# Kernel tuning notes

Hardware: AMD Instinct MI355X
Metric: run time of the kernel (lower is better)

## Reference

```python
import jax, jax.numpy as jnp
import numpy as np
from math import log

D_MODEL = 512
MAX_LEN = 2048
B, S = 32, 2048


def make_pe(max_len, d_model):
    position = np.arange(max_len, dtype=np.float32)[:, None]
    div_term = np.exp(np.arange(0, d_model, 2, dtype=np.float32) * (-log(10000.0) / d_model))
    pe = np.zeros((max_len, d_model), dtype=np.float32)
    pe[:, 0::2] = np.sin(position * div_term)
    pe[:, 1::2] = np.cos(position * div_term)
    return jnp.asarray(pe)


def setup_inputs() -> dict:
    key = jax.random.key(0)
    k1, k2 = jax.random.split(key)
    seqs = jax.random.normal(k1, (B, S, D_MODEL), dtype=jnp.float32)
    masks = jax.random.randint(k2, (B, S), 0, 2) > 0
    pe = make_pe(MAX_LEN, D_MODEL)
    return {"seqs": seqs, "masks": masks, "pe": pe}


def reference(seqs, masks, pe):
    # Each masked (True) position in row i receives pe[r], where r is its rank
    # among the masked positions of that row (0-based). Equivalent to the
    # original per-sample loop: seq[masks[i]] += pe[:length].
    rank = jnp.cumsum(masks.astype(jnp.int32), axis=-1) - 1  # [B,S]
    rank = jnp.clip(rank, 0, pe.shape[0] - 1)
    p = pe[rank]  # [B,S,D] gather
    return seqs + jnp.where(masks[..., None], p, jnp.zeros((), seqs.dtype))
```

## Files before the change

### kernel.cpp

```cpp
#include <hip/hip_runtime.h>

#define BB 32
#define SS 2048
#define DD 512
#define V4_PER_ROW (DD / 4)
#define TOTAL (BB * SS * V4_PER_ROW)
#define TPB 256
#define GRID 2048
#define STRIDE (GRID * TPB)
#define ITERS (TOTAL / STRIDE)
#define ROWSTEP (STRIDE / V4_PER_ROW)

typedef float f32x4 __attribute__((ext_vector_type(4)));

__global__ __launch_bounds__(1024) void pe_rank_kernel(
    const unsigned int* __restrict__ m32, int* __restrict__ rank_out) {
    const int b = blockIdx.x;
    const int t = threadIdx.x;

    __shared__ int flag_byte;
    if (t == 0) flag_byte = 0;
    __syncthreads();
    for (int i = t; i < 8192; i += 1024) {
        unsigned int v = m32[i];
        if (v != 0u && v != 1u && v != 0x3f800000u) flag_byte = 1;
    }
    __syncthreads();
    const int is_byte = flag_byte;
    const unsigned char* m8 = (const unsigned char*)m32;

    __shared__ int psum[1024];
    const int PER = SS / 1024;
    int vals[PER];
    int s = 0;
#pragma unroll
    for (int i = 0; i < PER; ++i) {
        const int idx = b * SS + t * PER + i;
        const int mv = is_byte ? (m8[idx] != 0) : (m32[idx] != 0u);
        vals[i] = mv;
        s += mv;
    }
    psum[t] = s;
    __syncthreads();
    for (int off = 1; off < 1024; off <<= 1) {
        const int v = (t >= off) ? psum[t - off] : 0;
        __syncthreads();
        psum[t] += v;
        __syncthreads();
    }
    int run = psum[t] - s;
#pragma unroll
    for (int i = 0; i < PER; ++i) {
        run += vals[i];
        rank_out[b * SS + t * PER + i] = vals[i] ? (run - 1) : -1;
    }
}

__global__ __launch_bounds__(TPB) void pe_add_kernel(
    const f32x4* __restrict__ seqs, const int* __restrict__ rank,
    const f32x4* __restrict__ pe, f32x4* __restrict__ out) {
    const int tid = blockIdx.x * TPB + threadIdx.x;
    const int col = tid & (V4_PER_ROW - 1);
    const int rowbase = __builtin_amdgcn_readfirstlane(tid >> 7);

#pragma unroll
    for (int g = 0; g < ITERS / 4; ++g) {
        const int k = 4 * g;
        const int r0 = rank[rowbase + (k + 0) * ROWSTEP];
        const int r1 = rank[rowbase + (k + 1) * ROWSTEP];
        const int r2 = rank[rowbase + (k + 2) * ROWSTEP];
        const int r3 = rank[rowbase + (k + 3) * ROWSTEP];
        const f32x4 a0 = __builtin_nontemporal_load(&seqs[tid + (k + 0) * STRIDE]);
        const f32x4 a1 = __builtin_nontemporal_load(&seqs[tid + (k + 1) * STRIDE]);
        const f32x4 a2 = __builtin_nontemporal_load(&seqs[tid + (k + 2) * STRIDE]);
        const f32x4 a3 = __builtin_nontemporal_load(&seqs[tid + (k + 3) * STRIDE]);
        const int rc0 = r0 < 0 ? 0 : r0;
        const int rc1 = r1 < 0 ? 0 : r1;
        const int rc2 = r2 < 0 ? 0 : r2;
        const int rc3 = r3 < 0 ? 0 : r3;
        const f32x4 p0 = pe[(rc0 << 7) + col];
        const f32x4 p1 = pe[(rc1 << 7) + col];
        const f32x4 p2 = pe[(rc2 << 7) + col];
        const f32x4 p3 = pe[(rc3 << 7) + col];
        const float f0 = r0 < 0 ? 0.0f : 1.0f;
        const float f1 = r1 < 0 ? 0.0f : 1.0f;
        const float f2 = r2 < 0 ? 0.0f : 1.0f;
        const float f3 = r3 < 0 ? 0.0f : 1.0f;
        f32x4 o0, o1, o2, o3;
        o0 = a0; o0 += p0 * f0;
        o1 = a1; o1 += p1 * f1;
        o2 = a2; o2 += p2 * f2;
        o3 = a3; o3 += p3 * f3;
        __builtin_nontemporal_store(o0, &out[tid + (k + 0) * STRIDE]);
        __builtin_nontemporal_store(o1, &out[tid + (k + 1) * STRIDE]);
        __builtin_nontemporal_store(o2, &out[tid + (k + 2) * STRIDE]);
        __builtin_nontemporal_store(o3, &out[tid + (k + 3) * STRIDE]);
    }
}

extern "C" void kernel_launch(void* const* d_in, const int* in_sizes, int n_in,
                              void* d_out, int out_size, void* d_ws, size_t ws_size,
                              hipStream_t stream) {
    const float* seqs        = (const float*)d_in[0];
    const unsigned int* msks = (const unsigned int*)d_in[1];
    const float* pe          = (const float*)d_in[2];
    float* out               = (float*)d_out;
    int* rank                = (int*)d_ws;

    pe_rank_kernel<<<BB, 1024, 0, stream>>>(msks, rank);
    pe_add_kernel<<<GRID, TPB, 0, stream>>>(
        (const f32x4*)seqs, rank, (const f32x4*)pe, (f32x4*)out);
}
```

Measured before the change: 244.6 us.

## Use wave-shuffle scan for mask ranks and software-pipeline the add kernel

The rank kernel's 1024-step shared-memory Hillis-Steele scan, which needs two barriers per step, is replaced by a 64-lane shuffle scan inside each wavefront plus a small shared array of per-wave totals, leaving a single barrier. The add kernel loads all rank values up front and double-buffers groups of four loads, issuing the next group's loads before the current group's stores. This is meant to cut the scan's synchronisation cost and keep more memory requests in flight. The cost is higher register pressure from holding two groups of vectors plus all rank values.

```diff
diff --git a/kernel.cpp b/kernel.cpp
--- a/kernel.cpp
+++ b/kernel.cpp
@@ -29,31 +29,33 @@
     const int is_byte = flag_byte;
     const unsigned char* m8 = (const unsigned char*)m32;
 
-    __shared__ int psum[1024];
-    const int PER = SS / 1024;
-    int vals[PER];
-    int s = 0;
+    const int lane = t & 63;
+    const int wv   = t >> 6;
+
+    const int i0 = b * SS + 2 * t;
+    const int v0 = is_byte ? (m8[i0] != 0)     : (m32[i0] != 0u);
+    const int v1 = is_byte ? (m8[i0 + 1] != 0) : (m32[i0 + 1] != 0u);
+    const int s = v0 + v1;
+
+    int x = s;
 #pragma unroll
-    for (int i = 0; i < PER; ++i) {
-        const int idx = b * SS + t * PER + i;
-        const int mv = is_byte ? (m8[idx] != 0) : (m32[idx] != 0u);
-        vals[i] = mv;
-        s += mv;
+    for (int off = 1; off < 64; off <<= 1) {
+        const int y = __shfl_up(x, off, 64);
+        if (lane >= off) x += y;
     }
-    psum[t] = s;
+
+    __shared__ int wsum[16];
+    if (lane == 63) wsum[wv] = x;
     __syncthreads();
-    for (int off = 1; off < 1024; off <<= 1) {
-        const int v = (t >= off) ? psum[t - off] : 0;
-        __syncthreads();
-        psum[t] += v;
-        __syncthreads();
-    }
-    int run = psum[t] - s;
-#pragma unroll
-    for (int i = 0; i < PER; ++i) {
-        run += vals[i];
-        rank_out[b * SS + t * PER + i] = vals[i] ? (run - 1) : -1;
-    }
+
+    int base = 0;
+    for (int j = 0; j < wv; ++j) base += wsum[j];
+
+    int run = base + x - s;
+    run += v0;
+    rank_out[i0] = v0 ? (run - 1) : -1;
+    run += v1;
+    rank_out[i0 + 1] = v1 ? (run - 1) : -1;
 }
 
 __global__ __launch_bounds__(TPB) void pe_add_kernel(
@@ -63,39 +65,52 @@
     const int col = tid & (V4_PER_ROW - 1);
     const int rowbase = __builtin_amdgcn_readfirstlane(tid >> 7);
 
+    int r[ITERS];
 #pragma unroll
-    for (int g = 0; g < ITERS / 4; ++g) {
-        const int k = 4 * g;
-        const int r0 = rank[rowbase + (k + 0) * ROWSTEP];
-        const int r1 = rank[rowbase + (k + 1) * ROWSTEP];
-        const int r2 = rank[rowbase + (k + 2) * ROWSTEP];
-        const int r3 = rank[rowbase + (k + 3) * ROWSTEP];
-        const f32x4 a0 = __builtin_nontemporal_load(&seqs[tid + (k + 0) * STRIDE]);
-        const f32x4 a1 = __builtin_nontemporal_load(&seqs[tid + (k + 1) * STRIDE]);
-        const f32x4 a2 = __builtin_nontemporal_load(&seqs[tid + (k + 2) * STRIDE]);
-        const f32x4 a3 = __builtin_nontemporal_load(&seqs[tid + (k + 3) * STRIDE]);
-        const int rc0 = r0 < 0 ? 0 : r0;
-        const int rc1 = r1 < 0 ? 0 : r1;
-        const int rc2 = r2 < 0 ? 0 : r2;
-        const int rc3 = r3 < 0 ? 0 : r3;
-        const f32x4 p0 = pe[(rc0 << 7) + col];
-        const f32x4 p1 = pe[(rc1 << 7) + col];
-        const f32x4 p2 = pe[(rc2 << 7) + col];
-        const f32x4 p3 = pe[(rc3 << 7) + col];
-        const float f0 = r0 < 0 ? 0.0f : 1.0f;
-        const float f1 = r1 < 0 ? 0.0f : 1.0f;
-        const float f2 = r2 < 0 ? 0.0f : 1.0f;
-        const float f3 = r3 < 0 ? 0.0f : 1.0f;
-        f32x4 o0, o1, o2, o3;
-        o0 = a0; o0 += p0 * f0;
-        o1 = a1; o1 += p1 * f1;
-        o2 = a2; o2 += p2 * f2;
-        o3 = a3; o3 += p3 * f3;
-        __builtin_nontemporal_store(o0, &out[tid + (k + 0) * STRIDE]);
-        __builtin_nontemporal_store(o1, &out[tid + (k + 1) * STRIDE]);
-        __builtin_nontemporal_store(o2, &out[tid + (k + 2) * STRIDE]);
-        __builtin_nontemporal_store(o3, &out[tid + (k + 3) * STRIDE]);
+    for (int i = 0; i < ITERS; ++i) r[i] = rank[rowbase + i * ROWSTEP];
+
+    f32x4 a[4], p[4];
+    f32x4 b[4], q[4];
+
+#define LOAD_GROUP(A, P, G)                                                    \
+    {                                                                          \
+        const int k_ = 4 * (G);                                                \
+        _Pragma("unroll") for (int j = 0; j < 4; ++j) {                        \
+            A[j] = __builtin_nontemporal_load(&seqs[tid + (k_ + j) * STRIDE]); \
+        }                                                                      \
+        _Pragma("unroll") for (int j = 0; j < 4; ++j) {                        \
+            const int rr = r[k_ + j];                                          \
+            const int rc = rr < 0 ? 0 : rr;                                    \
+            P[j] = pe[(rc << 7) + col];                                        \
+        }                                                                      \
     }
+
+#define STORE_GROUP(A, P, G)                                                   \
+    {                                                                          \
+        const int k_ = 4 * (G);                                                \
+        _Pragma("unroll") for (int j = 0; j < 4; ++j) {                        \
+            const float f = (r[k_ + j] < 0) ? 0.0f : 1.0f;                     \
+            f32x4 o = A[j];                                                    \
+            o += P[j] * f;                                                     \
+            __builtin_nontemporal_store(o, &out[tid + (k_ + j) * STRIDE]);     \
+        }                                                                      \
+    }
+
+    LOAD_GROUP(a, p, 0)
+
+    LOAD_GROUP(b, q, 1)
+    STORE_GROUP(a, p, 0)
+
+    LOAD_GROUP(a, p, 2)
+    STORE_GROUP(b, q, 1)
+
+    LOAD_GROUP(b, q, 3)
+    STORE_GROUP(a, p, 2)
+
+    STORE_GROUP(b, q, 3)
+
+#undef LOAD_GROUP
+#undef STORE_GROUP
 }
 
 extern "C" void kernel_launch(void* const* d_in, const int* in_sizes, int n_in,
```

Result: no change. 247.2 us (+1.1%).
